# Optimization experiments

Measured on AMD Instinct MI355X. Metric: run time of the kernel, lower is better.

Reference implementation:

```python
import jax, jax.numpy as jnp
import numpy as np

M0, M1 = 16, 16          # n_modes
C = 64                   # hidden_channels
B = 16                   # batch
H = W = 128              # spatial resolution
SCALE = C ** (-2)        # matches torch: scale * torch.rand(...)


def setup_inputs() -> dict:
    key = jax.random.key(0)
    kx, k0r, k0i, k1r, k1i = jax.random.split(key, 5)
    X = jax.random.normal(kx, (B, C, H, W), dtype=jnp.float32)
    wshape = (C, C, M0, M1)
    # torch.rand with cfloat draws U[0,1) for real and imag parts independently
    w0r = SCALE * jax.random.uniform(k0r, wshape, dtype=jnp.float32)
    w0i = SCALE * jax.random.uniform(k0i, wshape, dtype=jnp.float32)
    w1r = SCALE * jax.random.uniform(k1r, wshape, dtype=jnp.float32)
    w1i = SCALE * jax.random.uniform(k1i, wshape, dtype=jnp.float32)
    return {"X": X, "w0r": w0r, "w0i": w0i, "w1r": w1r, "w1i": w1i}


def reference(X, w0r, w0i, w1r, w1i):
    w0 = w0r + 1j * w0i                       # linear0: (C, C, M0, M1) complex
    w1 = w1r + 1j * w1i                       # linear1
    Xf = jnp.fft.rfftn(X, axes=(-2, -1), norm="forward")   # (B, C, H, W//2+1) complex
    # out[b,c] = sum_t weight[c,t] * Xf[b,t] on the two kept-mode corners
    top = jnp.einsum("ctxy,btxy->bcxy", w0, Xf[:, :, :M0, :M1])
    bot = jnp.einsum("ctxy,btxy->bcxy", w1, Xf[:, :, -M0:, :M1])
    Y = jnp.zeros_like(Xf)
    Y = Y.at[:, :, :M0, :M1].set(top)
    Y = Y.at[:, :, -M0:, :M1].set(bot)
    out = jnp.fft.irfftn(Y, axes=(-2, -1), s=(H, W), norm="forward")
    return out.astype(jnp.float32)
```

## Files before the change

### kernel.cpp

```cpp
#include <hip/hip_runtime.h>

#define PI2 6.28318530717958647692f

__global__ __launch_bounds__(256) void k_fwd(const float* __restrict__ X,
                                             float* __restrict__ Xf) {
  __shared__ __attribute__((aligned(16))) float E1t[64 * 32 * 2];
  __shared__ __attribute__((aligned(16))) float A2t[128 * 34 * 2];
  __shared__ __attribute__((aligned(16))) float E2t[64 * 16 * 2];
  const int plane = blockIdx.x;
  const int tid = threadIdx.x;
  const float* Xp = X + (size_t)plane * (128 * 128);

  #pragma unroll
  for (int k = 0; k < 8; ++k) {
    int idx = tid + k * 256;
    int h = idx >> 5, kxi = idx & 31;
    int kx = kxi + ((kxi >> 4) ? 96 : 0);
    float ang = -PI2 * (float)((kx * h) & 127) / 128.f;
    float s_, c_;
    __sincosf(ang, &s_, &c_);
    E1t[idx * 2] = c_; E1t[idx * 2 + 1] = s_;
  }
  #pragma unroll
  for (int k = 0; k < 4; ++k) {
    int idx = tid + k * 256;
    int w = idx >> 4, ky = idx & 15;
    float ang = -PI2 * (float)((ky * w) & 127) / 128.f;
    float s_, c_;
    __sincosf(ang, &s_, &c_);
    E2t[idx * 2] = c_; E2t[idx * 2 + 1] = s_;
  }
  __syncthreads();

  {
    const int w = tid & 127;
    const int kxg = tid >> 7;
    float cr[16], ci[16];
    #pragma unroll
    for (int j = 0; j < 16; ++j) { cr[j] = 0.f; ci[j] = 0.f; }
    float x0 = Xp[w], x1 = Xp[64 * 128 + w];
    for (int h = 0; h < 64; ++h) {
      float nx0 = 0.f, nx1 = 0.f;
      if (h < 63) { nx0 = Xp[(h + 1) * 128 + w]; nx1 = Xp[(h + 65) * 128 + w]; }
      float ue = x0 + x1;
      float uo = x0 - x1;
      const float4* Erow = (const float4*)&E1t[(h * 32 + kxg * 16) * 2];
      #pragma unroll
      for (int j2 = 0; j2 < 8; ++j2) {
        float4 e = Erow[j2];
        cr[2 * j2]     = fmaf(ue, e.x, cr[2 * j2]);
        ci[2 * j2]     = fmaf(ue, e.y, ci[2 * j2]);
        cr[2 * j2 + 1] = fmaf(uo, e.z, cr[2 * j2 + 1]);
        ci[2 * j2 + 1] = fmaf(uo, e.w, ci[2 * j2 + 1]);
      }
      x0 = nx0; x1 = nx1;
    }
    #pragma unroll
    for (int j = 0; j < 16; ++j) {
      int f2i = w * 34 + kxg * 16 + j;
      A2t[f2i * 2] = cr[j]; A2t[f2i * 2 + 1] = ci[j];
    }
  }
  __syncthreads();

  {
    const int kxi = tid >> 3;
    const int t = tid & 7;
    const float s = (t & 1) ? -1.f : 1.f;
    float r0 = 0.f, i0 = 0.f, r1 = 0.f, i1 = 0.f;
    for (int w = 0; w < 64; ++w) {
      const float2 a = *(const float2*)&A2t[(w * 34 + kxi) * 2];
      const float2 b = *(const float2*)&A2t[((w + 64) * 34 + kxi) * 2];
      float ur = fmaf(s, b.x, a.x);
      float ui = fmaf(s, b.y, a.y);
      const float2 e0 = *(const float2*)&E2t[(w * 16 + t) * 2];
      const float2 e1 = *(const float2*)&E2t[(w * 16 + t + 8) * 2];
      r0 = fmaf(ur, e0.x, r0); r0 = fmaf(-ui, e0.y, r0);
      i0 = fmaf(ur, e0.y, i0); i0 = fmaf(ui, e0.x, i0);
      r1 = fmaf(ur, e1.x, r1); r1 = fmaf(-ui, e1.y, r1);
      i1 = fmaf(ur, e1.y, i1); i1 = fmaf(ui, e1.x, i1);
    }
    const float sc = 1.f / 16384.f;
    float* base = Xf + (size_t)plane * 1024 + kxi * 32;
    *(float2*)&base[t * 2]       = make_float2(r0 * sc, i0 * sc);
    *(float2*)&base[(t + 8) * 2] = make_float2(r1 * sc, i1 * sc);
  }
}

__global__ __launch_bounds__(256) void k_mix(const float* __restrict__ Xf,
                                             const float* __restrict__ w0r,
                                             const float* __restrict__ w0i,
                                             const float* __restrict__ w1r,
                                             const float* __restrict__ w1i,
                                             float* __restrict__ Y) {
  __shared__ __attribute__((aligned(16))) float Wl[4 * 64 * 16 * 2];
  const int bid = blockIdx.x;
  const int c2 = bid >> 8;
  const int x  = (bid >> 4) & 15;
  const int cg = bid & 15;
  const int c0 = cg * 4;
  const int kxi = c2 * 16 + x;
  const float* Wr_g = c2 ? w1r : w0r;
  const float* Wi_g = c2 ? w1i : w0i;
  const int tid = threadIdx.x;
  const int b = tid >> 4;
  const int y = tid & 15;

  #pragma unroll
  for (int k = 0; k < 16; ++k) {
    int idx = tid + k * 256;
    int y_ = idx & 15, t_ = (idx >> 4) & 63, c_ = idx >> 10;
    size_t ga = (((size_t)(c0 + c_) * 64 + t_) * 16 + x) * 16 + y_;
    float wr = Wr_g[ga], wi = Wi_g[ga];
    Wl[idx * 2] = wr; Wl[idx * 2 + 1] = wi;
  }
  __syncthreads();

  float aR[4] = {}, aI[4] = {};
  const float* xbase = Xf + ((size_t)b * 64) * 1024 + kxi * 32 + y * 2;
  for (int t4 = 0; t4 < 64; t4 += 4) {
    float2 xv[4];
    #pragma unroll
    for (int q = 0; q < 4; ++q)
      xv[q] = *(const float2*)&xbase[(size_t)(t4 + q) * 1024];
    #pragma unroll
    for (int q = 0; q < 4; ++q) {
      int t = t4 + q;
      #pragma unroll
      for (int cj = 0; cj < 4; ++cj) {
        const float2 wv = *(const float2*)&Wl[((cj * 64 + t) * 16 + y) * 2];
        aR[cj] = fmaf(xv[q].x, wv.x, aR[cj]);
        aR[cj] = fmaf(-xv[q].y, wv.y, aR[cj]);
        aI[cj] = fmaf(xv[q].x, wv.y, aI[cj]);
        aI[cj] = fmaf(xv[q].y, wv.x, aI[cj]);
      }
    }
  }
  #pragma unroll
  for (int cj = 0; cj < 4; ++cj) {
    size_t ya = ((size_t)(b * 64 + c0 + cj)) * 1024 + kxi * 32 + y * 2;
    *(float2*)&Y[ya] = make_float2(aR[cj], aI[cj]);
  }
}

__global__ __launch_bounds__(256) void k_inv(const float* __restrict__ Y,
                                             float* __restrict__ out) {
  __shared__ __attribute__((aligned(16))) float Yl[1024];
  __shared__ __attribute__((aligned(16))) float Ml[128 * 18 * 2];
  const int plane = blockIdx.x;
  const int tid = threadIdx.x;
  {
    *(float4*)&Yl[tid * 4] = *(const float4*)&Y[(size_t)plane * 1024 + tid * 4];
  }
  __syncthreads();

  {
    const int g = tid >> 7;
    const int h = tid & 127;
    float zr[8] = {}, zi[8] = {};
    float uw, uwi;
    __sincosf(PI2 * (float)h / 128.f, &uwi, &uw);
    const float4* Yl4 = (const float4*)Yl;
    float Tr = 1.f, Ti = 0.f;
    #pragma unroll 4
    for (int kxi = 0; kxi < 16; ++kxi) {
      #pragma unroll
      for (int q = 0; q < 4; ++q) {
        float4 p = Yl4[kxi * 8 + g * 4 + q];
        int m = 2 * q;
        zr[m]   = fmaf(p.x, Tr, zr[m]);   zr[m]   = fmaf(-p.y, Ti, zr[m]);
        zi[m]   = fmaf(p.x, Ti, zi[m]);   zi[m]   = fmaf(p.y, Tr, zi[m]);
        zr[m+1] = fmaf(p.z, Tr, zr[m+1]); zr[m+1] = fmaf(-p.w, Ti, zr[m+1]);
        zi[m+1] = fmaf(p.z, Ti, zi[m+1]); zi[m+1] = fmaf(p.w, Tr, zi[m+1]);
      }
      float nr = Tr * uw - Ti * uwi, ni = Tr * uwi + Ti * uw;
      Tr = nr; Ti = ni;
    }
    __sincosf(PI2 * (float)((112 * h) & 127) / 128.f, &Ti, &Tr);
    #pragma unroll 4
    for (int kxi = 16; kxi < 32; ++kxi) {
      #pragma unroll
      for (int q = 0; q < 4; ++q) {
        float4 p = Yl4[kxi * 8 + g * 4 + q];
        int m = 2 * q;
        zr[m]   = fmaf(p.x, Tr, zr[m]);   zr[m]   = fmaf(-p.y, Ti, zr[m]);
        zi[m]   = fmaf(p.x, Ti, zi[m]);   zi[m]   = fmaf(p.y, Tr, zi[m]);
        zr[m+1] = fmaf(p.z, Tr, zr[m+1]); zr[m+1] = fmaf(-p.w, Ti, zr[m+1]);
        zi[m+1] = fmaf(p.z, Ti, zi[m+1]); zi[m+1] = fmaf(p.w, Tr, zi[m+1]);
      }
      float nr = Tr * uw - Ti * uwi, ni = Tr * uwi + Ti * uw;
      Tr = nr; Ti = ni;
    }
    #pragma unroll
    for (int m = 0; m < 8; ++m) {
      int ky = g * 8 + m;
      float f = (ky == 0) ? 1.f : 2.f;
      int f2i = h * 18 + ky;
      Ml[f2i * 2]     =  f * zr[m];
      Ml[f2i * 2 + 1] = -f * zi[m];
    }
  }
  __syncthreads();

  {
    const int hq = tid >> 6;
    const int w = tid & 63;
    float C[16], S[16];
    {
      float cw, sw;
      __sincosf(PI2 * (float)w / 128.f, &sw, &cw);
      C[0] = 1.f; S[0] = 0.f;
      #pragma unroll
      for (int k = 1; k < 16; ++k) {
        C[k] = C[k - 1] * cw - S[k - 1] * sw;
        S[k] = C[k - 1] * sw + S[k - 1] * cw;
      }
    }
    float* op = out + (size_t)plane * (128 * 128);
    const float4* Ml4 = (const float4*)Ml;
    for (int hj = 0; hj < 32; ++hj) {
      int h = hq * 32 + hj;
      float e = 0.f, o = 0.f;
      #pragma unroll
      for (int j2 = 0; j2 < 8; ++j2) {
        float4 m01 = Ml4[h * 9 + j2];
        int k = 2 * j2;
        float t0 = m01.x * C[k] + m01.y * S[k];
        float t1 = m01.z * C[k + 1] + m01.w * S[k + 1];
        e += t0; o += t1;
      }
      op[h * 128 + w]      = e + o;
      op[h * 128 + w + 64] = e - o;
    }
  }
}

extern "C" void kernel_launch(void* const* d_in, const int* in_sizes, int n_in,
                              void* d_out, int out_size, void* d_ws, size_t ws_size,
                              hipStream_t stream) {
  const float* X   = (const float*)d_in[0];
  const float* w0r = (const float*)d_in[1];
  const float* w0i = (const float*)d_in[2];
  const float* w1r = (const float*)d_in[3];
  const float* w1i = (const float*)d_in[4];
  float* outp = (float*)d_out;
  float* Xf = (float*)d_ws;
  float* Yw = (float*)d_ws + (1u << 20);
  k_fwd<<<1024, 256, 0, stream>>>(X, Xf);
  k_mix<<<512, 256, 0, stream>>>(Xf, w0r, w0i, w1r, w1i, Yw);
  k_inv<<<1024, 256, 0, stream>>>(Yw, outp);
}
```

Measured before the change: 183.4 us.

## Exploit DFT symmetries in forward and inverse transforms, repack mix weights

The forward row DFT now computes only 16 unique kx rows, using conjugate symmetry of real input to derive the negative frequencies, and replaces the column twiddle table with recurrence-generated twiddles. The inverse transform uses even/odd kx parity to produce two h rows per pass and quarter-period symmetry in w to produce four output columns per pass. The swizzled LDS layout is meant to avoid bank conflicts. Mix weights are packed as pairs so they load as float4, and occupancy hints are added. Together these cut FLOPs and LDS traffic, at the cost of some rounding drift from the twiddle recurrences.

Result: faster. 165.7 us (-9.7%).

```diff
diff --git a/kernel.cpp b/kernel.cpp
--- a/kernel.cpp
+++ b/kernel.cpp
@@ -2,63 +2,69 @@
 
 #define PI2 6.28318530717958647692f
 
-__global__ __launch_bounds__(256) void k_fwd(const float* __restrict__ X,
-                                             float* __restrict__ Xf) {
-  __shared__ __attribute__((aligned(16))) float E1t[64 * 32 * 2];
-  __shared__ __attribute__((aligned(16))) float A2t[128 * 34 * 2];
-  __shared__ __attribute__((aligned(16))) float E2t[64 * 16 * 2];
+__global__ __launch_bounds__(256, 4) void k_fwd(const float* __restrict__ X,
+                                                float* __restrict__ Xf) {
+  __shared__ __attribute__((aligned(16))) float A2t[128 * 18 * 2];
+  __shared__ __attribute__((aligned(16))) float Tt[64 * 16 * 2];
   const int plane = blockIdx.x;
   const int tid = threadIdx.x;
   const float* Xp = X + (size_t)plane * (128 * 128);
 
   #pragma unroll
-  for (int k = 0; k < 8; ++k) {
+  for (int k = 0; k < 4; ++k) {
     int idx = tid + k * 256;
-    int h = idx >> 5, kxi = idx & 31;
-    int kx = kxi + ((kxi >> 4) ? 96 : 0);
+    int h = idx >> 4, slot = idx & 15;
+    int kx = slot ? slot : 16;
     float ang = -PI2 * (float)((kx * h) & 127) / 128.f;
     float s_, c_;
     __sincosf(ang, &s_, &c_);
-    E1t[idx * 2] = c_; E1t[idx * 2 + 1] = s_;
-  }
-  #pragma unroll
-  for (int k = 0; k < 4; ++k) {
-    int idx = tid + k * 256;
-    int w = idx >> 4, ky = idx & 15;
-    float ang = -PI2 * (float)((ky * w) & 127) / 128.f;
-    float s_, c_;
-    __sincosf(ang, &s_, &c_);
-    E2t[idx * 2] = c_; E2t[idx * 2 + 1] = s_;
-  }
-  __syncthreads();
-
-  {
-    const int w = tid & 127;
-    const int kxg = tid >> 7;
-    float cr[16], ci[16];
-    #pragma unroll
-    for (int j = 0; j < 16; ++j) { cr[j] = 0.f; ci[j] = 0.f; }
-    float x0 = Xp[w], x1 = Xp[64 * 128 + w];
+    Tt[idx * 2] = c_; Tt[idx * 2 + 1] = s_;
+  }
+  __syncthreads();
+
+  {
+    const int w2 = tid & 63;
+    const int kxq = tid >> 6;
+    float ar[4][2], ai[4][2];
+    #pragma unroll
+    for (int j = 0; j < 4; ++j) {
+      ar[j][0] = 0.f; ar[j][1] = 0.f; ai[j][0] = 0.f; ai[j][1] = 0.f;
+    }
+    float dcA = 0.f, dcB = 0.f;
+    float x0a = Xp[w2],      x1a = Xp[64 * 128 + w2];
+    float x0b = Xp[w2 + 64], x1b = Xp[64 * 128 + w2 + 64];
     for (int h = 0; h < 64; ++h) {
-      float nx0 = 0.f, nx1 = 0.f;
-      if (h < 63) { nx0 = Xp[(h + 1) * 128 + w]; nx1 = Xp[(h + 65) * 128 + w]; }
-      float ue = x0 + x1;
-      float uo = x0 - x1;
-      const float4* Erow = (const float4*)&E1t[(h * 32 + kxg * 16) * 2];
-      #pragma unroll
-      for (int j2 = 0; j2 < 8; ++j2) {
-        float4 e = Erow[j2];
-        cr[2 * j2]     = fmaf(ue, e.x, cr[2 * j2]);
-        ci[2 * j2]     = fmaf(ue, e.y, ci[2 * j2]);
-        cr[2 * j2 + 1] = fmaf(uo, e.z, cr[2 * j2 + 1]);
-        ci[2 * j2 + 1] = fmaf(uo, e.w, ci[2 * j2 + 1]);
-      }
-      x0 = nx0; x1 = nx1;
-    }
-    #pragma unroll
-    for (int j = 0; j < 16; ++j) {
-      int f2i = w * 34 + kxg * 16 + j;
-      A2t[f2i * 2] = cr[j]; A2t[f2i * 2 + 1] = ci[j];
+      float n0a = 0.f, n1a = 0.f, n0b = 0.f, n1b = 0.f;
+      if (h < 63) {
+        n0a = Xp[(h + 1) * 128 + w2];      n1a = Xp[(h + 65) * 128 + w2];
+        n0b = Xp[(h + 1) * 128 + w2 + 64]; n1b = Xp[(h + 65) * 128 + w2 + 64];
+      }
+      float uea = x0a + x1a, uoa = x0a - x1a;
+      float ueb = x0b + x1b, uob = x0b - x1b;
+      const float4* Trow = (const float4*)&Tt[h * 32];
+      float4 e01 = Trow[kxq * 2];
+      float4 e23 = Trow[kxq * 2 + 1];
+      ar[0][0] = fmaf(uea, e01.x, ar[0][0]); ai[0][0] = fmaf(uea, e01.y, ai[0][0]);
+      ar[0][1] = fmaf(ueb, e01.x, ar[0][1]); ai[0][1] = fmaf(ueb, e01.y, ai[0][1]);
+      ar[1][0] = fmaf(uoa, e01.z, ar[1][0]); ai[1][0] = fmaf(uoa, e01.w, ai[1][0]);
+      ar[1][1] = fmaf(uob, e01.z, ar[1][1]); ai[1][1] = fmaf(uob, e01.w, ai[1][1]);
+      ar[2][0] = fmaf(uea, e23.x, ar[2][0]); ai[2][0] = fmaf(uea, e23.y, ai[2][0]);
+      ar[2][1] = fmaf(ueb, e23.x, ar[2][1]); ai[2][1] = fmaf(ueb, e23.y, ai[2][1]);
+      ar[3][0] = fmaf(uoa, e23.z, ar[3][0]); ai[3][0] = fmaf(uoa, e23.w, ai[3][0]);
+      ar[3][1] = fmaf(uob, e23.z, ar[3][1]); ai[3][1] = fmaf(uob, e23.w, ai[3][1]);
+      if (kxq == 0) { dcA += uea; dcB += ueb; }
+      x0a = n0a; x1a = n1a; x0b = n0b; x1b = n1b;
+    }
+    #pragma unroll
+    for (int j = 0; j < 4; ++j) {
+      int s = kxq * 4 + j;
+      int row = (s == 0) ? 16 : s;
+      *(float2*)&A2t[(w2 * 18 + row) * 2]        = make_float2(ar[j][0], ai[j][0]);
+      *(float2*)&A2t[((w2 + 64) * 18 + row) * 2] = make_float2(ar[j][1], ai[j][1]);
+    }
+    if (kxq == 0) {
+      *(float2*)&A2t[(w2 * 18) * 2]        = make_float2(dcA, 0.f);
+      *(float2*)&A2t[((w2 + 64) * 18) * 2] = make_float2(dcB, 0.f);
     }
   }
   __syncthreads();
@@ -66,19 +72,33 @@
   {
     const int kxi = tid >> 3;
     const int t = tid & 7;
+    const int row = (kxi < 16) ? kxi : (32 - kxi);
+    const float csign = (kxi < 16) ? 1.f : -1.f;
     const float s = (t & 1) ? -1.f : 1.f;
+    float s0r, s0i, s1r, s1i;
+    __sincosf(-PI2 * (float)t / 128.f, &s0i, &s0r);
+    __sincosf(-PI2 * (float)(t + 8) / 128.f, &s1i, &s1r);
     float r0 = 0.f, i0 = 0.f, r1 = 0.f, i1 = 0.f;
-    for (int w = 0; w < 64; ++w) {
-      const float2 a = *(const float2*)&A2t[(w * 34 + kxi) * 2];
-      const float2 b = *(const float2*)&A2t[((w + 64) * 34 + kxi) * 2];
-      float ur = fmaf(s, b.x, a.x);
-      float ui = fmaf(s, b.y, a.y);
-      const float2 e0 = *(const float2*)&E2t[(w * 16 + t) * 2];
-      const float2 e1 = *(const float2*)&E2t[(w * 16 + t + 8) * 2];
-      r0 = fmaf(ur, e0.x, r0); r0 = fmaf(-ui, e0.y, r0);
-      i0 = fmaf(ur, e0.y, i0); i0 = fmaf(ui, e0.x, i0);
-      r1 = fmaf(ur, e1.x, r1); r1 = fmaf(-ui, e1.y, r1);
-      i1 = fmaf(ur, e1.y, i1); i1 = fmaf(ui, e1.x, i1);
+    float E0r = 1.f, E0i = 0.f, E1r = 1.f, E1i = 0.f;
+    #pragma unroll
+    for (int half = 0; half < 2; ++half) {
+      if (half == 1) {
+        float c_, s_;
+        __sincosf(-1.57079632679489662f * (float)t, &s_, &c_);
+        E0r = c_; E0i = s_; E1r = c_; E1i = s_;
+      }
+      for (int w = half * 32; w < half * 32 + 32; ++w) {
+        float2 a = *(const float2*)&A2t[(w * 18 + row) * 2];
+        float2 b = *(const float2*)&A2t[((w + 64) * 18 + row) * 2];
+        float ur = fmaf(s, b.x, a.x);
+        float ui = csign * fmaf(s, b.y, a.y);
+        r0 = fmaf(ur, E0r, r0); r0 = fmaf(-ui, E0i, r0);
+        i0 = fmaf(ur, E0i, i0); i0 = fmaf(ui, E0r, i0);
+        r1 = fmaf(ur, E1r, r1); r1 = fmaf(-ui, E1i, r1);
+        i1 = fmaf(ur, E1i, i1); i1 = fmaf(ui, E1r, i1);
+        float u0 = E0r * s0r - E0i * s0i; E0i = E0r * s0i + E0i * s0r; E0r = u0;
+        float u1 = E1r * s1r - E1i * s1i; E1i = E1r * s1i + E1i * s1r; E1r = u1;
+      }
     }
     const float sc = 1.f / 16384.f;
     float* base = Xf + (size_t)plane * 1024 + kxi * 32;
@@ -87,13 +107,13 @@
   }
 }
 
-__global__ __launch_bounds__(256) void k_mix(const float* __restrict__ Xf,
-                                             const float* __restrict__ w0r,
-                                             const float* __restrict__ w0i,
-                                             const float* __restrict__ w1r,
-                                             const float* __restrict__ w1i,
-                                             float* __restrict__ Y) {
-  __shared__ __attribute__((aligned(16))) float Wl[4 * 64 * 16 * 2];
+__global__ __launch_bounds__(256, 2) void k_mix(const float* __restrict__ Xf,
+                                                const float* __restrict__ w0r,
+                                                const float* __restrict__ w0i,
+                                                const float* __restrict__ w1r,
+                                                const float* __restrict__ w1i,
+                                                float* __restrict__ Y) {
+  __shared__ __attribute__((aligned(16))) float Wl[4 * 32 * 16 * 4];
   const int bid = blockIdx.x;
   const int c2 = bid >> 8;
   const int x  = (bid >> 4) & 15;
@@ -111,28 +131,29 @@
     int idx = tid + k * 256;
     int y_ = idx & 15, t_ = (idx >> 4) & 63, c_ = idx >> 10;
     size_t ga = (((size_t)(c0 + c_) * 64 + t_) * 16 + x) * 16 + y_;
-    float wr = Wr_g[ga], wi = Wi_g[ga];
-    Wl[idx * 2] = wr; Wl[idx * 2 + 1] = wi;
+    int f2i = ((c_ * 32 + (t_ >> 1)) * 16 + y_) * 2 + (t_ & 1);
+    *(float2*)&Wl[f2i * 2] = make_float2(Wr_g[ga], Wi_g[ga]);
   }
   __syncthreads();
 
   float aR[4] = {}, aI[4] = {};
   const float* xbase = Xf + ((size_t)b * 64) * 1024 + kxi * 32 + y * 2;
-  for (int t4 = 0; t4 < 64; t4 += 4) {
-    float2 xv[4];
-    #pragma unroll
-    for (int q = 0; q < 4; ++q)
-      xv[q] = *(const float2*)&xbase[(size_t)(t4 + q) * 1024];
-    #pragma unroll
-    for (int q = 0; q < 4; ++q) {
-      int t = t4 + q;
+  for (int t8 = 0; t8 < 64; t8 += 8) {
+    float2 xv[8];
+    #pragma unroll
+    for (int q = 0; q < 8; ++q)
+      xv[q] = *(const float2*)&xbase[(size_t)(t8 + q) * 1024];
+    #pragma unroll
+    for (int p = 0; p < 4; ++p) {
+      int t2 = (t8 >> 1) + p;
+      float2 xe = xv[2 * p], xo = xv[2 * p + 1];
       #pragma unroll
       for (int cj = 0; cj < 4; ++cj) {
-        const float2 wv = *(const float2*)&Wl[((cj * 64 + t) * 16 + y) * 2];
-        aR[cj] = fmaf(xv[q].x, wv.x, aR[cj]);
-        aR[cj] = fmaf(-xv[q].y, wv.y, aR[cj]);
-        aI[cj] = fmaf(xv[q].x, wv.y, aI[cj]);
-        aI[cj] = fmaf(xv[q].y, wv.x, aI[cj]);
+        float4 wv = *(const float4*)&Wl[((cj * 32 + t2) * 16 + y) * 4];
+        aR[cj] = fmaf(xe.x, wv.x, aR[cj]); aR[cj] = fmaf(-xe.y, wv.y, aR[cj]);
+        aI[cj] = fmaf(xe.x, wv.y, aI[cj]); aI[cj] = fmaf(xe.y, wv.x, aI[cj]);
+        aR[cj] = fmaf(xo.x, wv.z, aR[cj]); aR[cj] = fmaf(-xo.y, wv.w, aR[cj]);
+        aI[cj] = fmaf(xo.x, wv.w, aI[cj]); aI[cj] = fmaf(xo.y, wv.z, aI[cj]);
       }
     }
   }
@@ -143,72 +164,79 @@
   }
 }
 
-__global__ __launch_bounds__(256) void k_inv(const float* __restrict__ Y,
-                                             float* __restrict__ out) {
+__global__ __launch_bounds__(256, 4) void k_inv(const float* __restrict__ Y,
+                                                float* __restrict__ out) {
   __shared__ __attribute__((aligned(16))) float Yl[1024];
-  __shared__ __attribute__((aligned(16))) float Ml[128 * 18 * 2];
+  __shared__ __attribute__((aligned(16))) float Mt[128 * 16 * 2];
   const int plane = blockIdx.x;
   const int tid = threadIdx.x;
-  {
-    *(float4*)&Yl[tid * 4] = *(const float4*)&Y[(size_t)plane * 1024 + tid * 4];
-  }
-  __syncthreads();
-
-  {
-    const int g = tid >> 7;
-    const int h = tid & 127;
-    float zr[8] = {}, zi[8] = {};
+  *(float4*)&Yl[tid * 4] = *(const float4*)&Y[(size_t)plane * 1024 + tid * 4];
+  __syncthreads();
+
+  {
+    const int g = tid >> 6;
+    const int h2 = tid & 63;
+    float zr[2][4] = {}, zi[2][4] = {};
     float uw, uwi;
-    __sincosf(PI2 * (float)h / 128.f, &uwi, &uw);
+    __sincosf(PI2 * (float)h2 / 128.f, &uwi, &uw);
     const float4* Yl4 = (const float4*)Yl;
     float Tr = 1.f, Ti = 0.f;
-    #pragma unroll 4
+    #pragma unroll 2
     for (int kxi = 0; kxi < 16; ++kxi) {
-      #pragma unroll
-      for (int q = 0; q < 4; ++q) {
-        float4 p = Yl4[kxi * 8 + g * 4 + q];
-        int m = 2 * q;
-        zr[m]   = fmaf(p.x, Tr, zr[m]);   zr[m]   = fmaf(-p.y, Ti, zr[m]);
-        zi[m]   = fmaf(p.x, Ti, zi[m]);   zi[m]   = fmaf(p.y, Tr, zi[m]);
-        zr[m+1] = fmaf(p.z, Tr, zr[m+1]); zr[m+1] = fmaf(-p.w, Ti, zr[m+1]);
-        zi[m+1] = fmaf(p.z, Ti, zi[m+1]); zi[m+1] = fmaf(p.w, Tr, zi[m+1]);
+      float sgn = (kxi & 1) ? -1.f : 1.f;
+      #pragma unroll
+      for (int q = 0; q < 2; ++q) {
+        float4 p = Yl4[kxi * 8 + g * 2 + q];
+        float cr0 = p.x * Tr - p.y * Ti, ci0 = p.x * Ti + p.y * Tr;
+        float cr1 = p.z * Tr - p.w * Ti, ci1 = p.z * Ti + p.w * Tr;
+        zr[0][2*q]   += cr0; zi[0][2*q]   += ci0;
+        zr[0][2*q+1] += cr1; zi[0][2*q+1] += ci1;
+        zr[1][2*q]   = fmaf(sgn, cr0, zr[1][2*q]);   zi[1][2*q]   = fmaf(sgn, ci0, zi[1][2*q]);
+        zr[1][2*q+1] = fmaf(sgn, cr1, zr[1][2*q+1]); zi[1][2*q+1] = fmaf(sgn, ci1, zi[1][2*q+1]);
       }
       float nr = Tr * uw - Ti * uwi, ni = Tr * uwi + Ti * uw;
       Tr = nr; Ti = ni;
     }
-    __sincosf(PI2 * (float)((112 * h) & 127) / 128.f, &Ti, &Tr);
-    #pragma unroll 4
+    __sincosf(PI2 * (float)((112 * h2) & 127) / 128.f, &Ti, &Tr);
+    #pragma unroll 2
     for (int kxi = 16; kxi < 32; ++kxi) {
-      #pragma unroll
-      for (int q = 0; q < 4; ++q) {
-        float4 p = Yl4[kxi * 8 + g * 4 + q];
-        int m = 2 * q;
-        zr[m]   = fmaf(p.x, Tr, zr[m]);   zr[m]   = fmaf(-p.y, Ti, zr[m]);
-        zi[m]   = fmaf(p.x, Ti, zi[m]);   zi[m]   = fmaf(p.y, Tr, zi[m]);
-        zr[m+1] = fmaf(p.z, Tr, zr[m+1]); zr[m+1] = fmaf(-p.w, Ti, zr[m+1]);
-        zi[m+1] = fmaf(p.z, Ti, zi[m+1]); zi[m+1] = fmaf(p.w, Tr, zi[m+1]);
+      float sgn = (kxi & 1) ? -1.f : 1.f;
+      #pragma unroll
+      for (int q = 0; q < 2; ++q) {
+        float4 p = Yl4[kxi * 8 + g * 2 + q];
+        float cr0 = p.x * Tr - p.y * Ti, ci0 = p.x * Ti + p.y * Tr;
+        float cr1 = p.z * Tr - p.w * Ti, ci1 = p.z * Ti + p.w * Tr;
+        zr[0][2*q]   += cr0; zi[0][2*q]   += ci0;
+        zr[0][2*q+1] += cr1; zi[0][2*q+1] += ci1;
+        zr[1][2*q]   = fmaf(sgn, cr0, zr[1][2*q]);   zi[1][2*q]   = fmaf(sgn, ci0, zi[1][2*q]);
+        zr[1][2*q+1] = fmaf(sgn, cr1, zr[1][2*q+1]); zi[1][2*q+1] = fmaf(sgn, ci1, zi[1][2*q+1]);
       }
       float nr = Tr * uw - Ti * uwi, ni = Tr * uwi + Ti * uw;
       Tr = nr; Ti = ni;
     }
     #pragma unroll
-    for (int m = 0; m < 8; ++m) {
-      int ky = g * 8 + m;
-      float f = (ky == 0) ? 1.f : 2.f;
-      int f2i = h * 18 + ky;
-      Ml[f2i * 2]     =  f * zr[m];
-      Ml[f2i * 2 + 1] = -f * zi[m];
-    }
-  }
-  __syncthreads();
-
-  {
-    const int hq = tid >> 6;
-    const int w = tid & 63;
+    for (int hs = 0; hs < 2; ++hs) {
+      int h = h2 + hs * 64;
+      #pragma unroll
+      for (int q = 0; q < 2; ++q) {
+        int ky0 = g * 4 + 2 * q;
+        float f0 = (ky0 == 0) ? 1.f : 2.f;
+        float4 v = make_float4(f0 * zr[hs][2*q],   -f0 * zi[hs][2*q],
+                               2.f * zr[hs][2*q+1], -2.f * zi[hs][2*q+1]);
+        int f4i = h * 8 + ((g * 2 + q) ^ (h & 7));
+        *(float4*)&Mt[f4i * 4] = v;
+      }
+    }
+  }
+  __syncthreads();
+
+  {
+    const int hp = tid >> 5;
+    const int w2 = tid & 31;
     float C[16], S[16];
     {
       float cw, sw;
-      __sincosf(PI2 * (float)w / 128.f, &sw, &cw);
+      __sincosf(PI2 * (float)w2 / 128.f, &sw, &cw);
       C[0] = 1.f; S[0] = 0.f;
       #pragma unroll
       for (int k = 1; k < 16; ++k) {
@@ -217,20 +245,26 @@
       }
     }
     float* op = out + (size_t)plane * (128 * 128);
-    const float4* Ml4 = (const float4*)Ml;
-    for (int hj = 0; hj < 32; ++hj) {
-      int h = hq * 32 + hj;
-      float e = 0.f, o = 0.f;
-      #pragma unroll
-      for (int j2 = 0; j2 < 8; ++j2) {
-        float4 m01 = Ml4[h * 9 + j2];
-        int k = 2 * j2;
-        float t0 = m01.x * C[k] + m01.y * S[k];
-        float t1 = m01.z * C[k + 1] + m01.w * S[k + 1];
-        e += t0; o += t1;
-      }
-      op[h * 128 + w]      = e + o;
-      op[h * 128 + w + 64] = e - o;
+    const float4* Mt4 = (const float4*)Mt;
+    #pragma unroll 2
+    for (int hj = 0; hj < 16; ++hj) {
+      int h = hp * 16 + hj;
+      float e = 0.f, o = 0.f, e2 = 0.f, o2 = 0.f;
+      #pragma unroll
+      for (int j = 0; j < 8; ++j) {
+        float4 m = Mt4[h * 8 + (j ^ (h & 7))];
+        int k0 = 2 * j, k1 = 2 * j + 1;
+        e = fmaf(m.x, C[k0], e); e = fmaf(m.y, S[k0], e);
+        o = fmaf(m.z, C[k1], o); o = fmaf(m.w, S[k1], o);
+        if ((k0 & 2) == 0) { e2 = fmaf(m.x, C[k0], e2); e2 = fmaf(m.y, S[k0], e2); }
+        else               { e2 = fmaf(-m.x, C[k0], e2); e2 = fmaf(-m.y, S[k0], e2); }
+        if ((k1 & 2) == 0) { o2 = fmaf(m.w, C[k1], o2); o2 = fmaf(-m.z, S[k1], o2); }
+        else               { o2 = fmaf(-m.w, C[k1], o2); o2 = fmaf(m.z, S[k1], o2); }
+      }
+      op[h * 128 + w2]      = e + o;
+      op[h * 128 + w2 + 64] = e - o;
+      op[h * 128 + w2 + 32] = e2 + o2;
+      op[h * 128 + w2 + 96] = e2 - o2;
     }
   }
 }
```
